# Kernel tuning notes

Measured on AMD Instinct MI355X. Metric: run time of the kernel, lower is better.

## Reference

```python
import jax, jax.numpy as jnp
import numpy as np

H = 16
D_MODEL = 1024
B, S = 2, 2048
DH = D_MODEL // H


def setup_inputs() -> dict:
    key = jax.random.key(0)
    ks = jax.random.split(key, 12)
    std = 0.02
    q = jax.random.normal(ks[0], (B, S, D_MODEL), dtype=jnp.float32)
    k = jax.random.normal(ks[1], (B, S, D_MODEL), dtype=jnp.float32)
    v = jax.random.normal(ks[2], (B, S, D_MODEL), dtype=jnp.float32)
    # additive causal mask: 0 on/below diagonal, -1e9 above
    causal = jnp.tril(jnp.ones((S, S), dtype=bool))
    mask = jnp.where(causal, 0.0, -1e9).astype(jnp.float32)[None, None, :, :]
    def dense(kk):
        return (jax.random.normal(kk, (D_MODEL, D_MODEL), dtype=jnp.float32) * std,
                jnp.zeros((D_MODEL,), dtype=jnp.float32))
    Wq, bq = dense(ks[3])
    Wk, bk = dense(ks[4])
    Wv, bv = dense(ks[5])
    Wo, bo = dense(ks[6])
    return {"q": q, "k": k, "v": v, "mask": mask,
            "Wq": Wq, "bq": bq, "Wk": Wk, "bk": bk,
            "Wv": Wv, "bv": bv, "Wo": Wo, "bo": bo}


def reference(q, k, v, mask, Wq, bq, Wk, bk, Wv, bv, Wo, bo):
    b, s, d = q.shape
    def split_heads(x):  # [b,s,d] -> [b,h,s,dh]
        return x.reshape(b, s, H, DH).transpose(0, 2, 1, 3)
    qh = split_heads(q @ Wq + bq)
    kh = split_heads(k @ Wk + bk)
    vh = split_heads(v @ Wv + bv)
    scale = 1.0 / jnp.sqrt(jnp.asarray(DH, dtype=qh.dtype))
    scores = jnp.einsum('bhqd,bhkd->bhqk', qh, kh) * scale + mask
    weights = jax.nn.softmax(scores, axis=-1)
    ctx = jnp.einsum('bhqk,bhkd->bhqd', weights, vh)
    ctx = ctx.transpose(0, 2, 1, 3).reshape(b, s, d)
    return ctx @ Wo + bo
```

## Files before the change

### kernel.cpp

```cpp
#include <hip/hip_runtime.h>
#include <hip/hip_bf16.h>
#include <stdint.h>

typedef __bf16 bf16x8 __attribute__((ext_vector_type(8)));
typedef float  f32x4  __attribute__((ext_vector_type(4)));
typedef __hip_bfloat16 bf16_t;

#define D_MODEL 1024
#define NH 16
#define DH 64
#define BB 2
#define SS 2048
#define MTOT (BB*SS)
#define NQT (SS/64)

#define GBM 128
#define GBN 64
#define GBK 64

__global__ void cvt_qkv_kernel(const float* __restrict__ q, const float* __restrict__ k,
                               const float* __restrict__ v, bf16_t* __restrict__ dst) {
  const int n1v = MTOT * D_MODEL / 4;
  int tid = blockIdx.x * blockDim.x + threadIdx.x;
  int stride = gridDim.x * blockDim.x;
  for (int i = tid; i < 3 * n1v; i += stride) {
    int which = i / n1v;
    int j = i - which * n1v;
    const float4* src = (const float4*)(which == 0 ? q : (which == 1 ? k : v));
    float4 f = src[j];
    union { bf16_t h[4]; short4 s4; } u;
    u.h[0] = __float2bfloat16(f.x);
    u.h[1] = __float2bfloat16(f.y);
    u.h[2] = __float2bfloat16(f.z);
    u.h[3] = __float2bfloat16(f.w);
    ((short4*)dst)[(size_t)which * n1v + j] = u.s4;
  }
}

__global__ void transpose_w_kernel(const float* __restrict__ W0, const float* __restrict__ W1,
                                   const float* __restrict__ W2, const float* __restrict__ W3,
                                   bf16_t* __restrict__ WtAll) {
  __shared__ float tile[32][33];
  const int z = blockIdx.z;
  const float* W = (z == 0) ? W0 : (z == 1) ? W1 : (z == 2) ? W2 : W3;
  bf16_t* Wt = WtAll + (size_t)z * D_MODEL * D_MODEL;
  const int tx = threadIdx.x, ty = threadIdx.y;
  const int bx = blockIdx.x, by = blockIdx.y;
#pragma unroll
  for (int i = 0; i < 4; ++i)
    tile[ty + i * 8][tx] = W[(size_t)(by * 32 + ty + i * 8) * D_MODEL + bx * 32 + tx];
  __syncthreads();
#pragma unroll
  for (int i = 0; i < 4; ++i)
    Wt[(size_t)(bx * 32 + ty + i * 8) * D_MODEL + by * 32 + tx] =
        __float2bfloat16(tile[tx][ty + i * 8]);
}

__device__ __forceinline__ void g2lds16(const bf16_t* g, bf16_t* l) {
  __builtin_amdgcn_global_load_lds((__attribute__((address_space(1))) void*)(g),
                                   (__attribute__((address_space(3))) void*)(l), 16, 0, 0);
}

__device__ __forceinline__ void gemm_stage(const bf16_t* __restrict__ A,
                                           const bf16_t* __restrict__ Bt,
                                           bf16_t* As, bf16_t* Bs,
                                           int m0, int n0, int kt, int wv, int ln) {
  const int row8 = ln >> 3;
  const int col = (ln & 7) * 8;
#pragma unroll
  for (int c = 0; c < 6; ++c) {
    int chunk = wv * 6 + c;
    if (chunk < 16) {
      g2lds16(A + (size_t)(m0 + chunk * 8 + row8) * D_MODEL + kt * GBK + col,
              As + chunk * 8 * GBK);
    } else {
      g2lds16(Bt + (size_t)(n0 + (chunk - 16) * 8 + row8) * D_MODEL + kt * GBK + col,
              Bs + (chunk - 16) * 8 * GBK);
    }
  }
}

__device__ __forceinline__ void gemm_tile_mainloop(const bf16_t* __restrict__ A,
                                                   const bf16_t* __restrict__ Bt,
                                                   bf16_t* As, bf16_t* Bs,
                                                   int m0, int n0, f32x4 acc[4][2]) {
  const int tid = threadIdx.x;
  const int wv = tid >> 6, ln = tid & 63;
  const int wr = wv >> 1, wc = wv & 1;
  const int lr = ln & 15, lg = ln >> 4;

#pragma unroll
  for (int mi = 0; mi < 4; ++mi)
#pragma unroll
    for (int ni = 0; ni < 2; ++ni)
      acc[mi][ni] = (f32x4){0.f, 0.f, 0.f, 0.f};

  const int NT = D_MODEL / GBK;
  gemm_stage(A, Bt, As, Bs, m0, n0, 0, wv, ln);
  __syncthreads();

  int cur = 0;
  for (int kt = 0; kt < NT; ++kt) {
    if (kt + 1 < NT)
      gemm_stage(A, Bt, As + (cur ^ 1) * (GBM * GBK), Bs + (cur ^ 1) * (GBN * GBK),
                 m0, n0, kt + 1, wv, ln);
    const bf16_t* Ab = As + cur * (GBM * GBK);
    const bf16_t* Bb = Bs + cur * (GBN * GBK);
#pragma unroll
    for (int ks = 0; ks < 2; ++ks) {
      bf16x8 af[4], bfr[2];
#pragma unroll
      for (int mi = 0; mi < 4; ++mi)
        af[mi] = *(const bf16x8*)(Ab + (size_t)(wr * 64 + mi * 16 + lr) * GBK + ks * 32 + lg * 8);
#pragma unroll
      for (int ni = 0; ni < 2; ++ni)
        bfr[ni] = *(const bf16x8*)(Bb + (size_t)(wc * 32 + ni * 16 + lr) * GBK + ks * 32 + lg * 8);
#pragma unroll
      for (int mi = 0; mi < 4; ++mi)
#pragma unroll
        for (int ni = 0; ni < 2; ++ni)
          acc[mi][ni] = __builtin_amdgcn_mfma_f32_16x16x32_bf16(af[mi], bfr[ni], acc[mi][ni], 0, 0, 0);
    }
    __syncthreads();
    cur ^= 1;
  }
}

__global__ __launch_bounds__(256)
void qk_proj_kernel(const bf16_t* __restrict__ Aq, const bf16_t* __restrict__ Ak,
                    const bf16_t* __restrict__ WtAll,
                    const float* __restrict__ bq, const float* __restrict__ bk,
                    bf16_t* __restrict__ Qg, bf16_t* __restrict__ Kg) {
  __shared__ bf16_t As[2 * GBM * GBK];
  __shared__ bf16_t Bs[2 * GBN * GBK];
  const int z = blockIdx.z;
  const bf16_t* A = (z == 0) ? Aq : Ak;
  const bf16_t* Bt = WtAll + (size_t)z * D_MODEL * D_MODEL;
  const float* bias = (z == 0) ? bq : bk;
  bf16_t* Out = (z == 0) ? Qg : Kg;
  const float scale = (z == 0) ? 0.125f : 1.0f;
  const int m0 = blockIdx.y * GBM, n0 = blockIdx.x * GBN;

  f32x4 acc[4][2];
  gemm_tile_mainloop(A, Bt, As, Bs, m0, n0, acc);

  const int tid = threadIdx.x;
  const int wv = tid >> 6, ln = tid & 63;
  const int wr = wv >> 1, wc = wv & 1;
  const int lr = ln & 15, lg = ln >> 4;

#pragma unroll
  for (int mi = 0; mi < 4; ++mi) {
#pragma unroll
    for (int ni = 0; ni < 2; ++ni) {
      int ncol = n0 + wc * 32 + ni * 16 + lr;
      float bsv = bias[ncol];
#pragma unroll
      for (int j = 0; j < 4; ++j) {
        int mrow = m0 + wr * 64 + mi * 16 + lg * 4 + j;
        Out[(size_t)mrow * D_MODEL + ncol] = __float2bfloat16((acc[mi][ni][j] + bsv) * scale);
      }
    }
  }
}

__global__ __launch_bounds__(256)
void vt_proj_kernel(const bf16_t* __restrict__ Wtv, const bf16_t* __restrict__ Av,
                    const float* __restrict__ bv, bf16_t* __restrict__ Vt) {
  __shared__ bf16_t As[2 * GBM * GBK];
  __shared__ bf16_t Bs[2 * GBN * GBK];
  const int m0 = blockIdx.y * GBM, n0 = blockIdx.x * GBN;

  f32x4 acc[4][2];
  gemm_tile_mainloop(Wtv, Av, As, Bs, m0, n0, acc);

  const int tid = threadIdx.x;
  const int wv = tid >> 6, ln = tid & 63;
  const int wr = wv >> 1, wc = wv & 1;
  const int lr = ln & 15, lg = ln >> 4;

#pragma unroll
  for (int mi = 0; mi < 4; ++mi) {
#pragma unroll
    for (int ni = 0; ni < 2; ++ni) {
      int ncol = n0 + wc * 32 + ni * 16 + lr;
#pragma unroll
      for (int j = 0; j < 4; ++j) {
        int mrow = m0 + wr * 64 + mi * 16 + lg * 4 + j;
        Vt[(size_t)mrow * MTOT + ncol] = __float2bfloat16(acc[mi][ni][j] + bv[mrow]);
      }
    }
  }
}

__global__ __launch_bounds__(256)
void out_gemm_kernel(const bf16_t* __restrict__ Ctx, const bf16_t* __restrict__ Wto,
                     const float* __restrict__ bo, float* __restrict__ out) {
  __shared__ bf16_t As[2 * GBM * GBK];
  __shared__ bf16_t Bs[2 * GBN * GBK];
  const int m0 = blockIdx.y * GBM, n0 = blockIdx.x * GBN;

  f32x4 acc[4][2];
  gemm_tile_mainloop(Ctx, Wto, As, Bs, m0, n0, acc);

  const int tid = threadIdx.x;
  const int wv = tid >> 6, ln = tid & 63;
  const int wr = wv >> 1, wc = wv & 1;
  const int lr = ln & 15, lg = ln >> 4;

#pragma unroll
  for (int mi = 0; mi < 4; ++mi) {
#pragma unroll
    for (int ni = 0; ni < 2; ++ni) {
      int ncol = n0 + wc * 32 + ni * 16 + lr;
      float bsv = bo[ncol];
#pragma unroll
      for (int j = 0; j < 4; ++j) {
        int mrow = m0 + wr * 64 + mi * 16 + lg * 4 + j;
        out[(size_t)mrow * D_MODEL + ncol] = acc[mi][ni][j] + bsv;
      }
    }
  }
}

__device__ __forceinline__ uint32_t pack2bf(float a, float b) {
  union { __hip_bfloat16 h; unsigned short u; } ua, ub;
  ua.h = __float2bfloat16(a);
  ub.h = __float2bfloat16(b);
  return (uint32_t)ua.u | ((uint32_t)ub.u << 16);
}

#define PSTRIDE 44

__device__ __forceinline__ void attn_run(
    f32x4 acc_o[2][4], f32x4 acc_l[2], float m_run[2],
    const bf16x8 qf[2][2], const bf16_t* Kbase, const bf16_t* Vbase,
    uint32_t (*P32)[PSTRIDE], int q0, int t0, int t1, int lr, int lg, bf16x8 onesf) {
  bf16x8 kf_cur[2][4];
#pragma unroll
  for (int ks = 0; ks < 2; ++ks)
#pragma unroll
    for (int kb = 0; kb < 4; ++kb)
      kf_cur[ks][kb] = *(const bf16x8*)(Kbase + (size_t)(t0 * 64 + kb * 16 + lr) * D_MODEL + ks * 32 + lg * 8);

  for (int t = t0; t < t1; ++t) {
    const int kv0 = t * 64;
    f32x4 sc[2][4];
#pragma unroll
    for (int qi = 0; qi < 2; ++qi)
#pragma unroll
      for (int kb = 0; kb < 4; ++kb) sc[qi][kb] = (f32x4){0.f, 0.f, 0.f, 0.f};

    __builtin_amdgcn_s_setprio(1);
#pragma unroll
    for (int ks = 0; ks < 2; ++ks) {
#pragma unroll
      for (int kb = 0; kb < 4; ++kb) {
        sc[0][kb] = __builtin_amdgcn_mfma_f32_16x16x32_bf16(kf_cur[ks][kb], qf[0][ks], sc[0][kb], 0, 0, 0);
        sc[1][kb] = __builtin_amdgcn_mfma_f32_16x16x32_bf16(kf_cur[ks][kb], qf[1][ks], sc[1][kb], 0, 0, 0);
      }
    }
    __builtin_amdgcn_s_setprio(0);

    bf16x8 kf_nxt[2][4];
    if (t + 1 < t1) {
#pragma unroll
      for (int ks = 0; ks < 2; ++ks)
#pragma unroll
        for (int kb = 0; kb < 4; ++kb)
          kf_nxt[ks][kb] = *(const bf16x8*)(Kbase + (size_t)(kv0 + 64 + kb * 16 + lr) * D_MODEL + ks * 32 + lg * 8);
    }
    bf16x8 vf[2][4];
#pragma unroll
    for (int ks = 0; ks < 2; ++ks)
#pragma unroll
      for (int db = 0; db < 4; ++db)
        vf[ks][db] = *(const bf16x8*)(Vbase + (size_t)(db * 16 + lr) * MTOT + kv0 + ks * 32 + lg * 8);

    if (kv0 + 63 > q0) {
#pragma unroll
      for (int qi = 0; qi < 2; ++qi) {
        int qc = q0 + qi * 16 + lr;
#pragma unroll
        for (int kb = 0; kb < 4; ++kb)
#pragma unroll
          for (int r = 0; r < 4; ++r) {
            int kc = kv0 + kb * 16 + 4 * lg + r;
            if (kc > qc) sc[qi][kb][r] = -1e30f;
          }
      }
    }

#pragma unroll
    for (int qi = 0; qi < 2; ++qi) {
      float vm = sc[qi][0][0];
#pragma unroll
      for (int kb = 0; kb < 4; ++kb)
#pragma unroll
        for (int r = 0; r < 4; ++r) vm = fmaxf(vm, sc[qi][kb][r]);
      vm = fmaxf(vm, __shfl_xor(vm, 16, 64));
      vm = fmaxf(vm, __shfl_xor(vm, 32, 64));
      float mo = m_run[qi];
      float mn = fmaxf(mo, vm);
      float scl = __expf(mo - mn);
      m_run[qi] = mn;
#pragma unroll
      for (int kb = 0; kb < 4; ++kb)
#pragma unroll
        for (int hh = 0; hh < 2; ++hh) {
          float p0 = __expf(sc[qi][kb][2 * hh]     - mn);
          float p1 = __expf(sc[qi][kb][2 * hh + 1] - mn);
          P32[qi * 16 + lr][8 * kb + 2 * lg + hh] = pack2bf(p0, p1);
        }
#pragma unroll
      for (int r = 0; r < 4; ++r) acc_l[qi][r] *= scl;
#pragma unroll
      for (int db = 0; db < 4; ++db)
#pragma unroll
        for (int r = 0; r < 4; ++r) acc_o[qi][db][r] *= scl;
    }

    asm volatile("s_waitcnt lgkmcnt(0)" ::: "memory");
    __builtin_amdgcn_sched_barrier(0);

    bf16x8 pb[2][2];
#pragma unroll
    for (int qi = 0; qi < 2; ++qi)
#pragma unroll
      for (int ks = 0; ks < 2; ++ks)
        pb[qi][ks] = *(const bf16x8*)&P32[qi * 16 + lr][16 * ks + 4 * lg];

    __builtin_amdgcn_s_setprio(1);
#pragma unroll
    for (int ks = 0; ks < 2; ++ks) {
#pragma unroll
      for (int qi = 0; qi < 2; ++qi) {
        acc_l[qi] = __builtin_amdgcn_mfma_f32_16x16x32_bf16(onesf, pb[qi][ks], acc_l[qi], 0, 0, 0);
#pragma unroll
        for (int db = 0; db < 4; ++db)
          acc_o[qi][db] = __builtin_amdgcn_mfma_f32_16x16x32_bf16(vf[ks][db], pb[qi][ks], acc_o[qi][db], 0, 0, 0);
      }
    }
    __builtin_amdgcn_s_setprio(0);

    if (t + 1 < t1) {
#pragma unroll
      for (int ks = 0; ks < 2; ++ks)
#pragma unroll
        for (int kb = 0; kb < 4; ++kb)
          kf_cur[ks][kb] = kf_nxt[ks][kb];
    }
  }
}

__device__ __forceinline__ void attn_load_q(bf16x8 qf[2][2], const bf16_t* Qbase,
                                            int q0, int lr, int lg) {
#pragma unroll
  for (int qi = 0; qi < 2; ++qi)
#pragma unroll
    for (int ks = 0; ks < 2; ++ks)
      qf[qi][ks] = *(const bf16x8*)(Qbase + (size_t)(q0 + qi * 16 + lr) * D_MODEL + ks * 32 + lg * 8);
}

__device__ __forceinline__ void attn_init(f32x4 acc_o[2][4], f32x4 acc_l[2], float m_run[2]) {
#pragma unroll
  for (int qi = 0; qi < 2; ++qi) {
#pragma unroll
    for (int db = 0; db < 4; ++db) acc_o[qi][db] = (f32x4){0.f, 0.f, 0.f, 0.f};
    acc_l[qi] = (f32x4){0.f, 0.f, 0.f, 0.f};
    m_run[qi] = -1e30f;
  }
}

__device__ __forceinline__ void store_ctx_tile(
    uint32_t (*P32)[PSTRIDE], const f32x4 acc_o[2][4], const f32x4 acc_l[2],
    bf16_t* __restrict__ Ctx, int b, int h, int q0, int ln, int lr, int lg) {
#pragma unroll
  for (int qi = 0; qi < 2; ++qi) {
    float rl = 1.0f / acc_l[qi][0];
#pragma unroll
    for (int db = 0; db < 4; ++db)
#pragma unroll
      for (int hh = 0; hh < 2; ++hh)
        P32[qi * 16 + lr][8 * db + 2 * lg + hh] =
            pack2bf(acc_o[qi][db][2 * hh] * rl, acc_o[qi][db][2 * hh + 1] * rl);
  }
  asm volatile("s_waitcnt lgkmcnt(0)" ::: "memory");
  __builtin_amdgcn_sched_barrier(0);
#pragma unroll
  for (int c = 0; c < 4; ++c) {
    int row = (ln >> 2) + 16 * (c >> 1);
    int dwc = (ln & 3) * 4 + 16 * (c & 1);
    bf16x8 v = *(const bf16x8*)&P32[row][dwc];
    *(bf16x8*)(Ctx + (size_t)(b * SS + q0 + row) * D_MODEL + h * DH + dwc * 2) = v;
  }
}

__global__ __launch_bounds__(256)
void attn_kernel(const bf16_t* __restrict__ Qg, const bf16_t* __restrict__ Kg,
                 const bf16_t* __restrict__ Vt, bf16_t* __restrict__ Ctx) {
  __shared__ __align__(16) uint32_t P32[4][32][PSTRIDE];
  __shared__ __align__(16) float O_part[2][32][68];
  __shared__ float ml_part[2][32][2];
  const int bh = blockIdx.x;
  const int pp = blockIdx.y;
  const int b = bh >> 4, h = bh & 15;
  const int wv = threadIdx.x >> 6, ln = threadIdx.x & 63;
  const int lr = ln & 15, lg = ln >> 4;

  const int qt_lo = pp, qt_hi = NQT - 1 - pp;
  const int h0 = 16 - pp;
  const int rh = wv & 1;

  const size_t qkbase = (size_t)b * SS * D_MODEL + (size_t)h * DH;
  const bf16_t* Qbase = Qg + qkbase;
  const bf16_t* Kbase = Kg + qkbase;
  const bf16_t* Vbase = Vt + (size_t)(h * DH) * MTOT + b * SS;

  bf16x8 onesf;
#pragma unroll
  for (int j = 0; j < 8; ++j) onesf[j] = (__bf16)1.0f;

  bf16x8 qf[2][2];
  f32x4 acc_o[2][4];
  f32x4 acc_l[2];
  float m_run[2];
  const int q0_hi = qt_hi * 64 + rh * 32;

  if (wv < 2) {
    const int q0_lo = qt_lo * 64 + rh * 32;
    attn_load_q(qf, Qbase, q0_lo, lr, lg);
    attn_init(acc_o, acc_l, m_run);
    attn_run(acc_o, acc_l, m_run, qf, Kbase, Vbase, P32[wv], q0_lo, 0, pp + 1, lr, lg, onesf);
    store_ctx_tile(P32[wv], acc_o, acc_l, Ctx, b, h, q0_lo, ln, lr, lg);

    attn_load_q(qf, Qbase, q0_hi, lr, lg);
    attn_init(acc_o, acc_l, m_run);
    attn_run(acc_o, acc_l, m_run, qf, Kbase, Vbase, P32[wv], q0_hi, 0, h0, lr, lg, onesf);
  } else {
    attn_load_q(qf, Qbase, q0_hi, lr, lg);
    attn_init(acc_o, acc_l, m_run);
    attn_run(acc_o, acc_l, m_run, qf, Kbase, Vbase, P32[wv], q0_hi, h0, NQT - pp, lr, lg, onesf);
    const int pidx = wv - 2;
#pragma unroll
    for (int qi = 0; qi < 2; ++qi) {
#pragma unroll
      for (int db = 0; db < 4; ++db)
        *(f32x4*)&O_part[pidx][qi * 16 + lr][16 * db + 4 * lg] = acc_o[qi][db];
      if (lg == 0) {
        ml_part[pidx][qi * 16 + lr][0] = m_run[qi];
        ml_part[pidx][qi * 16 + lr][1] = acc_l[qi][0];
      }
    }
  }

  __syncthreads();

  if (wv < 2) {
#pragma unroll
    for (int qi = 0; qi < 2; ++qi) {
      float m1 = m_run[qi];
      float m2 = ml_part[wv][qi * 16 + lr][0];
      float mn = fmaxf(m1, m2);
      float a1 = __expf(m1 - mn);
      float a2 = __expf(m2 - mn);
      float l = a1 * acc_l[qi][0] + a2 * ml_part[wv][qi * 16 + lr][1];
#pragma unroll
      for (int db = 0; db < 4; ++db) {
        f32x4 po = *(const f32x4*)&O_part[wv][qi * 16 + lr][16 * db + 4 * lg];
#pragma unroll
        for (int r = 0; r < 4; ++r)
          acc_o[qi][db][r] = a1 * acc_o[qi][db][r] + a2 * po[r];
      }
      acc_l[qi] = (f32x4){l, l, l, l};
    }
    store_ctx_tile(P32[wv], acc_o, acc_l, Ctx, b, h, q0_hi, ln, lr, lg);
  }
}

extern "C" void kernel_launch(void* const* d_in, const int* in_sizes, int n_in,
                              void* d_out, int out_size, void* d_ws, size_t ws_size,
                              hipStream_t stream) {
  const float* q  = (const float*)d_in[0];
  const float* k  = (const float*)d_in[1];
  const float* v  = (const float*)d_in[2];
  const float* bq = (const float*)d_in[5];
  const float* bk = (const float*)d_in[7];
  const float* bv = (const float*)d_in[9];
  const float* bo = (const float*)d_in[11];
  const float* Wq = (const float*)d_in[4];
  const float* Wk = (const float*)d_in[6];
  const float* Wv = (const float*)d_in[8];
  const float* Wo = (const float*)d_in[10];
  float* out = (float*)d_out;

  char* w = (char*)d_ws;
  bf16_t* Aqkv  = (bf16_t*)(w);
  bf16_t* WtAll = (bf16_t*)(w + 25165824);
  bf16_t* Qg    = (bf16_t*)(w + 33554432);
  bf16_t* Kg    = (bf16_t*)(w + 41943040);
  bf16_t* Vt    = (bf16_t*)(w + 50331648);
  bf16_t* Ctx   = (bf16_t*)(w + 58720256);

  cvt_qkv_kernel<<<2048, 256, 0, stream>>>(q, k, v, Aqkv);
  transpose_w_kernel<<<dim3(32, 32, 4), dim3(32, 8), 0, stream>>>(Wq, Wk, Wv, Wo, WtAll);
  qk_proj_kernel<<<dim3(16, 32, 2), 256, 0, stream>>>(
      Aqkv, Aqkv + (size_t)MTOT * D_MODEL, WtAll, bq, bk, Qg, Kg);
  vt_proj_kernel<<<dim3(64, 8), 256, 0, stream>>>(
      WtAll + 2 * (size_t)D_MODEL * D_MODEL, Aqkv + 2 * (size_t)MTOT * D_MODEL, bv, Vt);
  attn_kernel<<<dim3(32, 16), 256, 0, stream>>>(Qg, Kg, Vt, Ctx);
  out_gemm_kernel<<<dim3(16, 32), 256, 0, stream>>>(
      Ctx, WtAll + 3 * (size_t)D_MODEL * D_MODEL, bo, out);
}
```

Baseline: 264.7 us.

## Merge Q/K/V projections into one launch with larger 256x64 tiles

New measurement: 283.7 us. +7.2%, slower.

```diff
diff --git a/kernel.cpp b/kernel.cpp
--- a/kernel.cpp
+++ b/kernel.cpp
@@ -17,6 +17,10 @@
 #define GBM 128
 #define GBN 64
 #define GBK 64
+
+#define PBM 256
+#define PBN 64
+#define PBK 64
 
 __global__ void cvt_qkv_kernel(const float* __restrict__ q, const float* __restrict__ k,
                                const float* __restrict__ v, bf16_t* __restrict__ dst) {
@@ -61,6 +65,97 @@
                                    (__attribute__((address_space(3))) void*)(l), 16, 0, 0);
 }
 
+__global__ __launch_bounds__(256)
+void proj_fused_kernel(const bf16_t* __restrict__ Aq, const bf16_t* __restrict__ Ak,
+                       const bf16_t* __restrict__ Av, const bf16_t* __restrict__ WtAll,
+                       const float* __restrict__ bq, const float* __restrict__ bk,
+                       const float* __restrict__ bv,
+                       bf16_t* __restrict__ Qg, bf16_t* __restrict__ Kg,
+                       bf16_t* __restrict__ Vt) {
+  __shared__ bf16_t As[PBM * PBK];
+  __shared__ bf16_t Bs[PBN * PBK];
+  const int bid = blockIdx.x;
+  int z, m0, n0;
+  const bf16_t *A, *Bt;
+  if (bid < 512) {
+    z = bid >> 8;
+    const int local = bid & 255;
+    m0 = (local >> 4) * PBM;
+    n0 = (local & 15) * PBN;
+    A  = (z == 0) ? Aq : Ak;
+    Bt = WtAll + (size_t)z * D_MODEL * D_MODEL;
+  } else {
+    z = 2;
+    const int local = bid - 512;
+    m0 = (local >> 6) * PBM;
+    n0 = (local & 63) * PBN;
+    A  = WtAll + 2 * (size_t)D_MODEL * D_MODEL;
+    Bt = Av;
+  }
+
+  const int tid = threadIdx.x;
+  const int wv = tid >> 6, ln = tid & 63;
+  const int lr = ln & 15, lg = ln >> 4;
+  const int row8 = ln >> 3, col = (ln & 7) * 8;
+
+  f32x4 acc[4][4];
+#pragma unroll
+  for (int mi = 0; mi < 4; ++mi)
+#pragma unroll
+    for (int ni = 0; ni < 4; ++ni)
+      acc[mi][ni] = (f32x4){0.f, 0.f, 0.f, 0.f};
+
+  for (int kt = 0; kt < D_MODEL / PBK; ++kt) {
+#pragma unroll
+    for (int c = 0; c < 10; ++c) {
+      int chunk = wv * 10 + c;
+      if (chunk < 32) {
+        g2lds16(A + (size_t)(m0 + chunk * 8 + row8) * D_MODEL + kt * PBK + col,
+                As + chunk * 512);
+      } else {
+        g2lds16(Bt + (size_t)(n0 + (chunk - 32) * 8 + row8) * D_MODEL + kt * PBK + col,
+                Bs + (chunk - 32) * 512);
+      }
+    }
+    __syncthreads();
+#pragma unroll
+    for (int ks = 0; ks < 2; ++ks) {
+      bf16x8 af[4], bfr[4];
+#pragma unroll
+      for (int mi = 0; mi < 4; ++mi)
+        af[mi] = *(const bf16x8*)(As + (size_t)(wv * 64 + mi * 16 + lr) * PBK + ks * 32 + lg * 8);
+#pragma unroll
+      for (int ni = 0; ni < 4; ++ni)
+        bfr[ni] = *(const bf16x8*)(Bs + (size_t)(ni * 16 + lr) * PBK + ks * 32 + lg * 8);
+#pragma unroll
+      for (int mi = 0; mi < 4; ++mi)
+#pragma unroll
+        for (int ni = 0; ni < 4; ++ni)
+          acc[mi][ni] = __builtin_amdgcn_mfma_f32_16x16x32_bf16(af[mi], bfr[ni], acc[mi][ni], 0, 0, 0);
+    }
+    __syncthreads();
+  }
+
+#pragma unroll
+  for (int mi = 0; mi < 4; ++mi) {
+#pragma unroll
+    for (int ni = 0; ni < 4; ++ni) {
+      int ncol = n0 + ni * 16 + lr;
+#pragma unroll
+      for (int j = 0; j < 4; ++j) {
+        int mrow = m0 + wv * 64 + mi * 16 + lg * 4 + j;
+        if (z == 0) {
+          Qg[(size_t)mrow * D_MODEL + ncol] = __float2bfloat16((acc[mi][ni][j] + bq[ncol]) * 0.125f);
+        } else if (z == 1) {
+          Kg[(size_t)mrow * D_MODEL + ncol] = __float2bfloat16(acc[mi][ni][j] + bk[ncol]);
+        } else {
+          Vt[(size_t)mrow * MTOT + ncol] = __float2bfloat16(acc[mi][ni][j] + bv[mrow]);
+        }
+      }
+    }
+  }
+}
+
 __device__ __forceinline__ void gemm_stage(const bf16_t* __restrict__ A,
                                            const bf16_t* __restrict__ Bt,
                                            bf16_t* As, bf16_t* Bs,
@@ -123,73 +218,6 @@
     }
     __syncthreads();
     cur ^= 1;
-  }
-}
-
-__global__ __launch_bounds__(256)
-void qk_proj_kernel(const bf16_t* __restrict__ Aq, const bf16_t* __restrict__ Ak,
-                    const bf16_t* __restrict__ WtAll,
-                    const float* __restrict__ bq, const float* __restrict__ bk,
-                    bf16_t* __restrict__ Qg, bf16_t* __restrict__ Kg) {
-  __shared__ bf16_t As[2 * GBM * GBK];
-  __shared__ bf16_t Bs[2 * GBN * GBK];
-  const int z = blockIdx.z;
-  const bf16_t* A = (z == 0) ? Aq : Ak;
-  const bf16_t* Bt = WtAll + (size_t)z * D_MODEL * D_MODEL;
-  const float* bias = (z == 0) ? bq : bk;
-  bf16_t* Out = (z == 0) ? Qg : Kg;
-  const float scale = (z == 0) ? 0.125f : 1.0f;
-  const int m0 = blockIdx.y * GBM, n0 = blockIdx.x * GBN;
-
-  f32x4 acc[4][2];
-  gemm_tile_mainloop(A, Bt, As, Bs, m0, n0, acc);
-
-  const int tid = threadIdx.x;
-  const int wv = tid >> 6, ln = tid & 63;
-  const int wr = wv >> 1, wc = wv & 1;
-  const int lr = ln & 15, lg = ln >> 4;
-
-#pragma unroll
-  for (int mi = 0; mi < 4; ++mi) {
-#pragma unroll
-    for (int ni = 0; ni < 2; ++ni) {
-      int ncol = n0 + wc * 32 + ni * 16 + lr;
-      float bsv = bias[ncol];
-#pragma unroll
-      for (int j = 0; j < 4; ++j) {
-        int mrow = m0 + wr * 64 + mi * 16 + lg * 4 + j;
-        Out[(size_t)mrow * D_MODEL + ncol] = __float2bfloat16((acc[mi][ni][j] + bsv) * scale);
-      }
-    }
-  }
-}
-
-__global__ __launch_bounds__(256)
-void vt_proj_kernel(const bf16_t* __restrict__ Wtv, const bf16_t* __restrict__ Av,
-                    const float* __restrict__ bv, bf16_t* __restrict__ Vt) {
-  __shared__ bf16_t As[2 * GBM * GBK];
-  __shared__ bf16_t Bs[2 * GBN * GBK];
-  const int m0 = blockIdx.y * GBM, n0 = blockIdx.x * GBN;
-
-  f32x4 acc[4][2];
-  gemm_tile_mainloop(Wtv, Av, As, Bs, m0, n0, acc);
-
-  const int tid = threadIdx.x;
-  const int wv = tid >> 6, ln = tid & 63;
-  const int wr = wv >> 1, wc = wv & 1;
-  const int lr = ln & 15, lg = ln >> 4;
-
-#pragma unroll
-  for (int mi = 0; mi < 4; ++mi) {
-#pragma unroll
-    for (int ni = 0; ni < 2; ++ni) {
-      int ncol = n0 + wc * 32 + ni * 16 + lr;
-#pragma unroll
-      for (int j = 0; j < 4; ++j) {
-        int mrow = m0 + wr * 64 + mi * 16 + lg * 4 + j;
-        Vt[(size_t)mrow * MTOT + ncol] = __float2bfloat16(acc[mi][ni][j] + bv[mrow]);
-      }
-    }
   }
 }
 
@@ -504,10 +532,9 @@
 
   cvt_qkv_kernel<<<2048, 256, 0, stream>>>(q, k, v, Aqkv);
   transpose_w_kernel<<<dim3(32, 32, 4), dim3(32, 8), 0, stream>>>(Wq, Wk, Wv, Wo, WtAll);
-  qk_proj_kernel<<<dim3(16, 32, 2), 256, 0, stream>>>(
-      Aqkv, Aqkv + (size_t)MTOT * D_MODEL, WtAll, bq, bk, Qg, Kg);
-  vt_proj_kernel<<<dim3(64, 8), 256, 0, stream>>>(
-      WtAll + 2 * (size_t)D_MODEL * D_MODEL, Aqkv + 2 * (size_t)MTOT * D_MODEL, bv, Vt);
+  proj_fused_kernel<<<768, 256, 0, stream>>>(
+      Aqkv, Aqkv + (size_t)MTOT * D_MODEL, Aqkv + 2 * (size_t)MTOT * D_MODEL,
+      WtAll, bq, bk, bv, Qg, Kg, Vt);
   attn_kernel<<<dim3(32, 16), 256, 0, stream>>>(Qg, Kg, Vt, Ctx);
   out_gemm_kernel<<<dim3(16, 32), 256, 0, stream>>>(
       Ctx, WtAll + 3 * (size_t)D_MODEL * D_MODEL, bo, out);
```
